# Performance work log

Hardware: AMD Instinct MI355X
Metric: run time of the kernel (lower is better)

The kernel has to match this reference:

```python
import jax, jax.numpy as jnp
import numpy as np

IN_F, OUT_F = 1024, 1024
NUM, K = 5, 3            # pykan defaults: num grid intervals, spline degree
X_RANGE = 1.0
LN_EPS = 1e-5
BATCH = 4096


def _make_grid():
    # pykan: linspace over [-R, R] with num+1 points, extended by k points of
    # uniform spacing h on each side -> (in_dim, num + 2k + 1)
    g = np.linspace(-X_RANGE, X_RANGE, NUM + 1)
    h = (g[-1] - g[0]) / NUM
    ext = np.concatenate([g[0] - h * np.arange(K, 0, -1), g, g[-1] + h * np.arange(1, K + 1)])
    grid = np.broadcast_to(ext, (IN_F, NUM + 2 * K + 1)).copy()
    return jnp.asarray(grid, dtype=jnp.float32)


def setup_inputs() -> dict:
    key = jax.random.key(0)
    ks = jax.random.split(key, 4)
    x = jax.random.uniform(ks[0], (BATCH, IN_F), jnp.float32, -1.0, 1.0)
    coef = jax.random.normal(ks[1], (IN_F, OUT_F, NUM + K), jnp.float32) * 0.1
    scale_base = jax.random.normal(ks[2], (IN_F, OUT_F), jnp.float32) / jnp.sqrt(jnp.float32(IN_F))
    scale_sp = jnp.ones((IN_F, OUT_F), jnp.float32)
    gamma = jnp.ones((OUT_F,), jnp.float32)   # LayerNorm weight
    beta = jnp.zeros((OUT_F,), jnp.float32)   # LayerNorm bias
    return {"x": x, "coef": coef, "scale_base": scale_base, "scale_sp": scale_sp,
            "gamma": gamma, "beta": beta, "grid": _make_grid()}


def _b_splines(x, grid, k):
    # Cox-de Boor recursion, exactly as pykan B_batch (uniform grid -> no NaNs).
    # x: (B, in), grid: (in, G) -> basis (B, in, NUM + k)
    xe = x[:, :, None]
    g = grid[None, :, :]
    B = ((xe >= g[:, :, :-1]) & (xe < g[:, :, 1:])).astype(x.dtype)
    for p in range(1, k + 1):
        B = ((xe - g[:, :, :-(p + 1)]) / (g[:, :, p:-1] - g[:, :, :-(p + 1)]) * B[:, :, :-1]
             + (g[:, :, p + 1:] - xe) / (g[:, :, p + 1:] - g[:, :, 1:-p]) * B[:, :, 1:])
    return B


def reference(x, coef, scale_base, scale_sp, gamma, beta, grid):
    basis = _b_splines(x, grid, K)                        # (B, in, NUM+K)
    spline = jnp.einsum('bik,iok->bio', basis, coef)      # (B, in, out)
    base = jax.nn.silu(x)                                 # (B, in)  pykan base_fun
    y = scale_base[None, :, :] * base[:, :, None] + scale_sp[None, :, :] * spline
    y = jnp.sum(y, axis=1)                                # (B, out)
    # LayerNorm(out_features)
    mu = jnp.mean(y, axis=-1, keepdims=True)
    var = jnp.var(y, axis=-1, keepdims=True)
    return (y - mu) * jax.lax.rsqrt(var + LN_EPS) * gamma + beta
```

## Files before the change

kernel.cpp:

```cpp
#include <hip/hip_runtime.h>

#define IN_F   1024
#define OUT_F  1024
#define BATCHN 4096
#define KDIM   9216

using i32x4 = __attribute__((ext_vector_type(4))) int;

__device__ __forceinline__ unsigned short f2bf(float f) {
  union { float f; unsigned int u; } v; v.f = f;
  unsigned int u = v.u;
  unsigned int r = (u + 0x7FFFu + ((u >> 16) & 1u)) >> 16;
  return (unsigned short)r;
}

__device__ __forceinline__ float bf2f(unsigned short h) {
  union { unsigned int u; float f; } v; v.u = ((unsigned int)h) << 16;
  return v.f;
}

#define ASCALE 172.0f

__device__ __forceinline__ unsigned char qa(float v) {
  return (unsigned char)(char)__float2int_rn(v * ASCALE);
}

__device__ __forceinline__ void async_load16(const void* g, void* l) {
  __builtin_amdgcn_global_load_lds(
      (__attribute__((address_space(1))) void*)(g),
      (__attribute__((address_space(3))) void*)(l),
      16, 0, 0);
}

__global__ __launch_bounds__(256) void kan_prep(const float* __restrict__ x,
                                                const float* __restrict__ grid,
                                                const float* __restrict__ sb,
                                                const float* __restrict__ ssp,
                                                const float* __restrict__ coef,
                                                unsigned char* __restrict__ A,
                                                unsigned int* __restrict__ sraw) {
  int bid = blockIdx.x;
  int tid = threadIdx.x;
  if (bid < 4096) {
    int idx4 = bid * 256 + tid;
    int b  = idx4 >> 8;
    int i0 = (idx4 & 255) * 4;
    const float4 xv4 = *(const float4*)(x + (size_t)b * IN_F + i0);
    const float4* gp = (const float4*)grid;
    float4 g0 = gp[0], g1 = gp[1], g2 = gp[2];
    float t[12] = {g0.x, g0.y, g0.z, g0.w, g1.x, g1.y, g1.z, g1.w,
                   g2.x, g2.y, g2.z, g2.w};
    float inv_h = 1.0f / (t[4] - t[3]);
    const float invp[3] = {inv_h, inv_h * 0.5f, inv_h * (1.0f / 3.0f)};
    float xs[4] = {xv4.x, xv4.y, xv4.z, xv4.w};
    unsigned char o9[9][4];
#pragma unroll
    for (int e = 0; e < 4; ++e) {
      float xv = xs[e];
      float sil = xv / (1.0f + __expf(-xv));
      float B[11];
#pragma unroll
      for (int j = 0; j < 11; ++j) B[j] = (xv >= t[j] && xv < t[j + 1]) ? 1.0f : 0.0f;
#pragma unroll
      for (int p = 1; p <= 3; ++p) {
        float ip = invp[p - 1];
#pragma unroll
        for (int j = 0; j + p < 11; ++j)
          B[j] = (xv - t[j]) * ip * B[j] + (t[j + p + 1] - xv) * ip * B[j + 1];
      }
      o9[0][e] = qa(sil);
#pragma unroll
      for (int k = 0; k < 8; ++k) o9[k + 1][e] = qa(B[k]);
    }
    size_t base = (size_t)b * KDIM + i0;
#pragma unroll
    for (int tp = 0; tp < 9; ++tp)
      *(unsigned int*)(A + base + (size_t)tp * 1024) = *(const unsigned int*)&o9[tp][0];
  } else {
    int b2 = bid - 4096;
    int o  = (b2 & 3) * 256 + tid;
    int ib = (b2 >> 2) * 32;
    float m = 0.f;
    for (int ii = 0; ii < 32; ++ii) {
      int io = (ib + ii) * 1024 + o;
      float s = ssp[io];
      float mm = fabsf(sb[io]);
      const float4* cp = (const float4*)(coef + (size_t)io * 8);
      float4 c0 = cp[0], c1 = cp[1];
      mm = fmaxf(mm, fmaxf(fmaxf(fabsf(s * c0.x), fabsf(s * c0.y)),
                           fmaxf(fabsf(s * c0.z), fabsf(s * c0.w))));
      mm = fmaxf(mm, fmaxf(fmaxf(fabsf(s * c1.x), fabsf(s * c1.y)),
                           fmaxf(fabsf(s * c1.z), fabsf(s * c1.w))));
      m = fmaxf(m, mm);
    }
    atomicMax(sraw + o, __float_as_uint(m));
  }
}

__global__ __launch_bounds__(256) void kan_prep_w(const float* __restrict__ sb,
                                                  const float* __restrict__ ssp,
                                                  const float* __restrict__ coef,
                                                  const unsigned int* __restrict__ sraw,
                                                  unsigned char* __restrict__ WT) {
  __shared__ unsigned char lds[9][128][33];
  int i0 = (blockIdx.x >> 5) * 128, o0 = (blockIdx.x & 31) * 32;
  int tid = threadIdx.x;
  int oo = tid & 31;
  float qs = 127.f / __uint_as_float(sraw[o0 + oo]);
#pragma unroll
  for (int r = 0; r < 16; ++r) {
    int idx = r * 256 + tid;
    int ii = idx >> 5;
    int io = (i0 + ii) * 1024 + (o0 + oo);
    float b = sb[io], s = ssp[io];
    const float4* cp = (const float4*)(coef + (size_t)io * 8);
    float4 c0 = cp[0], c1 = cp[1];
    lds[0][ii][oo] = (unsigned char)(char)__float2int_rn(b * qs);
    lds[1][ii][oo] = (unsigned char)(char)__float2int_rn(s * c0.x * qs);
    lds[2][ii][oo] = (unsigned char)(char)__float2int_rn(s * c0.y * qs);
    lds[3][ii][oo] = (unsigned char)(char)__float2int_rn(s * c0.z * qs);
    lds[4][ii][oo] = (unsigned char)(char)__float2int_rn(s * c0.w * qs);
    lds[5][ii][oo] = (unsigned char)(char)__float2int_rn(s * c1.x * qs);
    lds[6][ii][oo] = (unsigned char)(char)__float2int_rn(s * c1.y * qs);
    lds[7][ii][oo] = (unsigned char)(char)__float2int_rn(s * c1.z * qs);
    lds[8][ii][oo] = (unsigned char)(char)__float2int_rn(s * c1.w * qs);
  }
  __syncthreads();
  int woo = tid >> 3, ig = tid & 7;
  size_t rowbase = (size_t)(o0 + woo) * KDIM + i0 + ig * 16;
#pragma unroll
  for (int tp = 0; tp < 9; ++tp) {
    unsigned char tmp[16];
#pragma unroll
    for (int q = 0; q < 16; ++q) tmp[q] = lds[tp][ig * 16 + q][woo];
    *(uint4*)(WT + rowbase + (size_t)tp * 1024) = *(const uint4*)tmp;
  }
}

#define BM 256
#define BN 256
#define BKB 128
#define NSP 4
#define KQ   (KDIM / NSP)
#define NSLI (KQ / BKB)
#define SLOT 32768

__global__ __launch_bounds__(512, 2) void kan_gemm(const unsigned char* __restrict__ A,
                                                   const unsigned char* __restrict__ BT,
                                                   const unsigned int* __restrict__ sraw,
                                                   unsigned short* __restrict__ P) {
  extern __shared__ unsigned char lds[];
  unsigned char* As = lds;
  unsigned char* Bs = lds + 3 * SLOT;
  const int tid = threadIdx.x;
  const int wid = tid >> 6, lane = tid & 63;
  const int wr = wid >> 2, wc = wid & 3;
  const int row16 = lane & 15, kgrp = lane >> 4;
  const int rswB = (row16 & 7) << 4;

  int wg = ((blockIdx.x & 7) << 5) | (blockIdx.x >> 3);
  const int s = wg >> 6;
  const int m0 = ((wg >> 2) & 15) * BM, n0 = (wg & 3) * BN;
  const size_t kbase = (size_t)s * KQ;
  const unsigned char* Ab = A;
  const unsigned char* Bb = BT;

  i32x4 acc[8][4] = {};

  auto stage = [&](const unsigned char* Gb, int grow0, unsigned char* slotp, int sl) {
    size_t kbyte = kbase + (size_t)sl * BKB;
#pragma unroll
    for (int q = 0; q < 4; ++q) {
      int d = q * 8192 + tid * 16;
      int row = d >> 7;
      int csw = (d & 127) ^ ((row & 7) << 4);
      async_load16(Gb + (size_t)(grow0 + row) * KDIM + kbyte + csw,
                   slotp + (q * 8192 + wid * 1024));
    }
  };

  stage(Ab, m0, As, 0);
  stage(Bb, n0, Bs, 0);
  stage(Ab, m0, As + SLOT, 1);

  int consA = 0;
  for (int sl = 0; sl < NSLI; ++sl) {
    if (sl < NSLI - 1) asm volatile("s_waitcnt vmcnt(4)" ::: "memory");
    else               asm volatile("s_waitcnt vmcnt(0)" ::: "memory");
    __builtin_amdgcn_s_barrier();
    __builtin_amdgcn_sched_barrier(0);
    const unsigned char* as = As + consA * SLOT;
    const unsigned char* bs = Bs + (sl & 1) * SLOT;
    const int cb0 = (kgrp << 4) ^ rswB;
    const int cb1 = (64 | (kgrp << 4)) ^ rswB;

    i32x4 b0[4], a0[4];
#pragma unroll
    for (int n = 0; n < 4; ++n)
      b0[n] = *(const i32x4*)(bs + (wc * 64 + n * 16 + row16) * 128 + cb0);
#pragma unroll
    for (int m = 0; m < 4; ++m)
      a0[m] = *(const i32x4*)(as + (wr * 128 + m * 16 + row16) * 128 + cb0);
    if (sl + 1 < NSLI) stage(Bb, n0, Bs + ((sl + 1) & 1) * SLOT, sl + 1);
    __builtin_amdgcn_sched_barrier(0);
    __builtin_amdgcn_s_barrier();
    __builtin_amdgcn_s_setprio(1);
#pragma unroll
    for (int m = 0; m < 4; ++m)
#pragma unroll
      for (int n = 0; n < 4; ++n)
        acc[m][n] = __builtin_amdgcn_mfma_i32_16x16x64_i8(a0[m], b0[n], acc[m][n], 0, 0, 0);
    __builtin_amdgcn_s_setprio(0);

    i32x4 a1[4];
#pragma unroll
    for (int m = 0; m < 4; ++m)
      a1[m] = *(const i32x4*)(as + (wr * 128 + (m + 4) * 16 + row16) * 128 + cb0);
    {
      int stgA = consA - 1; if (stgA < 0) stgA += 3;
      if (sl + 2 < NSLI) stage(Ab, m0, As + stgA * SLOT, sl + 2);
    }
    __builtin_amdgcn_sched_barrier(0);
    __builtin_amdgcn_s_barrier();
    __builtin_amdgcn_s_setprio(1);
#pragma unroll
    for (int m = 0; m < 4; ++m)
#pragma unroll
      for (int n = 0; n < 4; ++n)
        acc[m + 4][n] = __builtin_amdgcn_mfma_i32_16x16x64_i8(a1[m], b0[n], acc[m + 4][n], 0, 0, 0);
    __builtin_amdgcn_s_setprio(0);

    i32x4 b1[4], a2[4];
#pragma unroll
    for (int n = 0; n < 4; ++n)
      b1[n] = *(const i32x4*)(bs + (wc * 64 + n * 16 + row16) * 128 + cb1);
#pragma unroll
    for (int m = 0; m < 4; ++m)
      a2[m] = *(const i32x4*)(as + (wr * 128 + m * 16 + row16) * 128 + cb1);
    __builtin_amdgcn_sched_barrier(0);
    __builtin_amdgcn_s_barrier();
    __builtin_amdgcn_s_setprio(1);
#pragma unroll
    for (int m = 0; m < 4; ++m)
#pragma unroll
      for (int n = 0; n < 4; ++n)
        acc[m][n] = __builtin_amdgcn_mfma_i32_16x16x64_i8(a2[m], b1[n], acc[m][n], 0, 0, 0);
    __builtin_amdgcn_s_setprio(0);

    i32x4 a3[4];
#pragma unroll
    for (int m = 0; m < 4; ++m)
      a3[m] = *(const i32x4*)(as + (wr * 128 + (m + 4) * 16 + row16) * 128 + cb1);
    __builtin_amdgcn_sched_barrier(0);
    __builtin_amdgcn_s_barrier();
    __builtin_amdgcn_s_setprio(1);
#pragma unroll
    for (int m = 0; m < 4; ++m)
#pragma unroll
      for (int n = 0; n < 4; ++n)
        acc[m + 4][n] = __builtin_amdgcn_mfma_i32_16x16x64_i8(a3[m], b1[n], acc[m + 4][n], 0, 0, 0);
    __builtin_amdgcn_s_setprio(0);

    consA = (consA == 2) ? 0 : consA + 1;
  }

  float dq[4];
#pragma unroll
  for (int n = 0; n < 4; ++n)
    dq[n] = __uint_as_float(sraw[n0 + wc * 64 + n * 16 + row16]) * (1.f / (ASCALE * 127.f));

  unsigned short* Pb = P + (size_t)s * BATCHN * OUT_F
                     + (size_t)(m0 + wr * 128) * OUT_F + n0 + wc * 64;
#pragma unroll
  for (int m = 0; m < 8; ++m)
#pragma unroll
    for (int n = 0; n < 4; ++n)
#pragma unroll
      for (int r = 0; r < 4; ++r)
        Pb[(size_t)(m * 16 + kgrp * 4 + r) * OUT_F + n * 16 + row16] =
            f2bf((float)acc[m][n][r] * dq[n]);
}

__global__ __launch_bounds__(256) void kan_ln(float* __restrict__ y,
                                              const unsigned short* __restrict__ P,
                                              const float* __restrict__ gamma,
                                              const float* __restrict__ beta) {
  __shared__ float ss[4], ssq[4];
  int tid = threadIdx.x;
  float4 v = {0.f, 0.f, 0.f, 0.f};
#pragma unroll
  for (int pp = 0; pp < NSP; ++pp) {
    const ushort4 pv = ((const ushort4*)(P + (size_t)pp * BATCHN * OUT_F
                                           + (size_t)blockIdx.x * OUT_F))[tid];
    v.x += bf2f(pv.x);
    v.y += bf2f(pv.y);
    v.z += bf2f(pv.z);
    v.w += bf2f(pv.w);
  }
  float s = v.x + v.y + v.z + v.w;
  float q = v.x * v.x + v.y * v.y + v.z * v.z + v.w * v.w;
#pragma unroll
  for (int off = 1; off < 64; off <<= 1) {
    s += __shfl_xor(s, off);
    q += __shfl_xor(q, off);
  }
  if ((tid & 63) == 0) { ss[tid >> 6] = s; ssq[tid >> 6] = q; }
  __syncthreads();
  float S = ss[0] + ss[1] + ss[2] + ss[3];
  float Q = ssq[0] + ssq[1] + ssq[2] + ssq[3];
  float mu  = S * (1.0f / OUT_F);
  float var = Q * (1.0f / OUT_F) - mu * mu;
  float inv = rsqrtf(var + 1e-5f);
  const float4 g  = ((const float4*)gamma)[tid];
  const float4 bt = ((const float4*)beta)[tid];
  float4 o;
  o.x = (v.x - mu) * inv * g.x + bt.x;
  o.y = (v.y - mu) * inv * g.y + bt.y;
  o.z = (v.z - mu) * inv * g.z + bt.z;
  o.w = (v.w - mu) * inv * g.w + bt.w;
  ((float4*)(y + (size_t)blockIdx.x * OUT_F))[tid] = o;
}

extern "C" void kernel_launch(void* const* d_in, const int* in_sizes, int n_in,
                              void* d_out, int out_size, void* d_ws, size_t ws_size,
                              hipStream_t stream) {
  const float* x     = (const float*)d_in[0];
  const float* coef  = (const float*)d_in[1];
  const float* sb    = (const float*)d_in[2];
  const float* ssp   = (const float*)d_in[3];
  const float* gamma = (const float*)d_in[4];
  const float* beta  = (const float*)d_in[5];
  const float* grid  = (const float*)d_in[6];

  const size_t a_bytes  = (size_t)BATCHN * KDIM;
  const size_t wt_bytes = (size_t)OUT_F * KDIM;
  const size_t sr_bytes = 4096;
  const size_t p_bytes  = (size_t)NSP * BATCHN * OUT_F * 2;
  if (ws_size < a_bytes + wt_bytes + sr_bytes + p_bytes) return;

  unsigned char* A    = (unsigned char*)d_ws;
  unsigned char* WT   = A + a_bytes;
  unsigned int*  sraw = (unsigned int*)(WT + wt_bytes);
  unsigned short* P   = (unsigned short*)((unsigned char*)sraw + sr_bytes);
  float* y = (float*)d_out;

  const size_t lds_bytes = 5 * (size_t)SLOT;
  static bool attr_set = false;
  if (!attr_set) {
    hipFuncSetAttribute((const void*)kan_gemm,
                        hipFuncAttributeMaxDynamicSharedMemorySize, (int)lds_bytes);
    attr_set = true;
  }

  hipMemsetAsync(sraw, 0, sr_bytes, stream);
  kan_prep<<<dim3(4096 + 128), dim3(256), 0, stream>>>(x, grid, sb, ssp, coef, A, sraw);
  kan_prep_w<<<dim3((IN_F / 128) * (OUT_F / 32)), dim3(256), 0, stream>>>(sb, ssp, coef, sraw, WT);
  kan_gemm<<<dim3(NSP * (BATCHN / BM) * (OUT_F / BN)), dim3(512), lds_bytes, stream>>>(A, WT, sraw, P);
  kan_ln<<<dim3(BATCHN), dim3(256), 0, stream>>>(y, P, gamma, beta);
}
```

Measured before the change: 93.50 us.

## Fuse per-column weight max reduction into weight quantization kernel, drop atomics

The column-wise max used for int8 weight scaling moves out of the combined prep kernel and into the weight-quantization kernel. Each 512-thread block now owns 8 output columns, reduces their max over all inputs through shared memory, then quantizes and writes the transposed rows directly without an LDS transpose. This removes the memset, the global atomicMax and the cross-kernel dependency on sraw, and splits activation prep into its own kernel. The cost is that the weight kernel now runs only 128 blocks, which may underuse the GPU's bandwidth. Each block also reads its weight slice twice, relying on cache reuse for the second pass.

```diff
diff --git a/kernel.cpp b/kernel.cpp
--- a/kernel.cpp
+++ b/kernel.cpp
@@ -32,109 +32,103 @@
       16, 0, 0);
 }
 
-__global__ __launch_bounds__(256) void kan_prep(const float* __restrict__ x,
-                                                const float* __restrict__ grid,
-                                                const float* __restrict__ sb,
-                                                const float* __restrict__ ssp,
-                                                const float* __restrict__ coef,
-                                                unsigned char* __restrict__ A,
-                                                unsigned int* __restrict__ sraw) {
-  int bid = blockIdx.x;
-  int tid = threadIdx.x;
-  if (bid < 4096) {
-    int idx4 = bid * 256 + tid;
-    int b  = idx4 >> 8;
-    int i0 = (idx4 & 255) * 4;
-    const float4 xv4 = *(const float4*)(x + (size_t)b * IN_F + i0);
-    const float4* gp = (const float4*)grid;
-    float4 g0 = gp[0], g1 = gp[1], g2 = gp[2];
-    float t[12] = {g0.x, g0.y, g0.z, g0.w, g1.x, g1.y, g1.z, g1.w,
-                   g2.x, g2.y, g2.z, g2.w};
-    float inv_h = 1.0f / (t[4] - t[3]);
-    const float invp[3] = {inv_h, inv_h * 0.5f, inv_h * (1.0f / 3.0f)};
-    float xs[4] = {xv4.x, xv4.y, xv4.z, xv4.w};
-    unsigned char o9[9][4];
-#pragma unroll
-    for (int e = 0; e < 4; ++e) {
-      float xv = xs[e];
-      float sil = xv / (1.0f + __expf(-xv));
-      float B[11];
-#pragma unroll
-      for (int j = 0; j < 11; ++j) B[j] = (xv >= t[j] && xv < t[j + 1]) ? 1.0f : 0.0f;
-#pragma unroll
-      for (int p = 1; p <= 3; ++p) {
-        float ip = invp[p - 1];
-#pragma unroll
-        for (int j = 0; j + p < 11; ++j)
-          B[j] = (xv - t[j]) * ip * B[j] + (t[j + p + 1] - xv) * ip * B[j + 1];
-      }
-      o9[0][e] = qa(sil);
-#pragma unroll
-      for (int k = 0; k < 8; ++k) o9[k + 1][e] = qa(B[k]);
+__global__ __launch_bounds__(256) void kan_prep_a(const float* __restrict__ x,
+                                                  const float* __restrict__ grid,
+                                                  unsigned char* __restrict__ A) {
+  int idx4 = blockIdx.x * 256 + threadIdx.x;
+  int b  = idx4 >> 8;
+  int i0 = (idx4 & 255) * 4;
+  const float4 xv4 = *(const float4*)(x + (size_t)b * IN_F + i0);
+  const float4* gp = (const float4*)grid;
+  float4 g0 = gp[0], g1 = gp[1], g2 = gp[2];
+  float t[12] = {g0.x, g0.y, g0.z, g0.w, g1.x, g1.y, g1.z, g1.w,
+                 g2.x, g2.y, g2.z, g2.w};
+  float inv_h = 1.0f / (t[4] - t[3]);
+  const float invp[3] = {inv_h, inv_h * 0.5f, inv_h * (1.0f / 3.0f)};
+  float xs[4] = {xv4.x, xv4.y, xv4.z, xv4.w};
+  unsigned char o9[9][4];
+#pragma unroll
+  for (int e = 0; e < 4; ++e) {
+    float xv = xs[e];
+    float sil = xv / (1.0f + __expf(-xv));
+    float B[11];
+#pragma unroll
+    for (int j = 0; j < 11; ++j) B[j] = (xv >= t[j] && xv < t[j + 1]) ? 1.0f : 0.0f;
+#pragma unroll
+    for (int p = 1; p <= 3; ++p) {
+      float ip = invp[p - 1];
+#pragma unroll
+      for (int j = 0; j + p < 11; ++j)
+        B[j] = (xv - t[j]) * ip * B[j] + (t[j + p + 1] - xv) * ip * B[j + 1];
     }
-    size_t base = (size_t)b * KDIM + i0;
-#pragma unroll
-    for (int tp = 0; tp < 9; ++tp)
-      *(unsigned int*)(A + base + (size_t)tp * 1024) = *(const unsigned int*)&o9[tp][0];
-  } else {
-    int b2 = bid - 4096;
-    int o  = (b2 & 3) * 256 + tid;
-    int ib = (b2 >> 2) * 32;
-    float m = 0.f;
-    for (int ii = 0; ii < 32; ++ii) {
-      int io = (ib + ii) * 1024 + o;
-      float s = ssp[io];
-      float mm = fabsf(sb[io]);
-      const float4* cp = (const float4*)(coef + (size_t)io * 8);
-      float4 c0 = cp[0], c1 = cp[1];
-      mm = fmaxf(mm, fmaxf(fmaxf(fabsf(s * c0.x), fabsf(s * c0.y)),
-                           fmaxf(fabsf(s * c0.z), fabsf(s * c0.w))));
-      mm = fmaxf(mm, fmaxf(fmaxf(fabsf(s * c1.x), fabsf(s * c1.y)),
-                           fmaxf(fabsf(s * c1.z), fabsf(s * c1.w))));
-      m = fmaxf(m, mm);
-    }
-    atomicMax(sraw + o, __float_as_uint(m));
-  }
-}
-
-__global__ __launch_bounds__(256) void kan_prep_w(const float* __restrict__ sb,
+    o9[0][e] = qa(sil);
+#pragma unroll
+    for (int k = 0; k < 8; ++k) o9[k + 1][e] = qa(B[k]);
+  }
+  size_t base = (size_t)b * KDIM + i0;
+#pragma unroll
+  for (int tp = 0; tp < 9; ++tp)
+    *(unsigned int*)(A + base + (size_t)tp * 1024) = *(const unsigned int*)&o9[tp][0];
+}
+
+__global__ __launch_bounds__(512) void kan_prep_w(const float* __restrict__ sb,
                                                   const float* __restrict__ ssp,
                                                   const float* __restrict__ coef,
-                                                  const unsigned int* __restrict__ sraw,
+                                                  unsigned int* __restrict__ sraw,
                                                   unsigned char* __restrict__ WT) {
-  __shared__ unsigned char lds[9][128][33];
-  int i0 = (blockIdx.x >> 5) * 128, o0 = (blockIdx.x & 31) * 32;
-  int tid = threadIdx.x;
-  int oo = tid & 31;
-  float qs = 127.f / __uint_as_float(sraw[o0 + oo]);
-#pragma unroll
-  for (int r = 0; r < 16; ++r) {
-    int idx = r * 256 + tid;
-    int ii = idx >> 5;
-    int io = (i0 + ii) * 1024 + (o0 + oo);
+  __shared__ float lmax[64][8];
+  __shared__ float qs8[8];
+  const int tid = threadIdx.x;
+  const int oo = tid & 7, ig = tid >> 3;
+  const int o = blockIdx.x * 8 + oo;
+  const int ibase = ig * 16;
+
+  float m = 0.f;
+#pragma unroll 4
+  for (int ii = 0; ii < 16; ++ii) {
+    int io = (ibase + ii) * 1024 + o;
+    float s = ssp[io];
+    float mm = fabsf(sb[io]);
+    const float4* cp = (const float4*)(coef + (size_t)io * 8);
+    float4 c0 = cp[0], c1 = cp[1];
+    mm = fmaxf(mm, fmaxf(fmaxf(fabsf(s * c0.x), fabsf(s * c0.y)),
+                         fmaxf(fabsf(s * c0.z), fabsf(s * c0.w))));
+    mm = fmaxf(mm, fmaxf(fmaxf(fabsf(s * c1.x), fabsf(s * c1.y)),
+                         fmaxf(fabsf(s * c1.z), fabsf(s * c1.w))));
+    m = fmaxf(m, mm);
+  }
+  lmax[ig][oo] = m;
+  __syncthreads();
+  if (tid < 8) {
+    float mo = 0.f;
+    for (int r = 0; r < 64; ++r) mo = fmaxf(mo, lmax[r][tid]);
+    sraw[blockIdx.x * 8 + tid] = __float_as_uint(mo);
+    qs8[tid] = 127.f / mo;
+  }
+  __syncthreads();
+  const float qs = qs8[oo];
+
+  unsigned char tmp[9][16];
+#pragma unroll
+  for (int ii = 0; ii < 16; ++ii) {
+    int io = (ibase + ii) * 1024 + o;
     float b = sb[io], s = ssp[io];
     const float4* cp = (const float4*)(coef + (size_t)io * 8);
     float4 c0 = cp[0], c1 = cp[1];
-    lds[0][ii][oo] = (unsigned char)(char)__float2int_rn(b * qs);
-    lds[1][ii][oo] = (unsigned char)(char)__float2int_rn(s * c0.x * qs);
-    lds[2][ii][oo] = (unsigned char)(char)__float2int_rn(s * c0.y * qs);
-    lds[3][ii][oo] = (unsigned char)(char)__float2int_rn(s * c0.z * qs);
-    lds[4][ii][oo] = (unsigned char)(char)__float2int_rn(s * c0.w * qs);
-    lds[5][ii][oo] = (unsigned char)(char)__float2int_rn(s * c1.x * qs);
-    lds[6][ii][oo] = (unsigned char)(char)__float2int_rn(s * c1.y * qs);
-    lds[7][ii][oo] = (unsigned char)(char)__float2int_rn(s * c1.z * qs);
-    lds[8][ii][oo] = (unsigned char)(char)__float2int_rn(s * c1.w * qs);
-  }
-  __syncthreads();
-  int woo = tid >> 3, ig = tid & 7;
-  size_t rowbase = (size_t)(o0 + woo) * KDIM + i0 + ig * 16;
-#pragma unroll
-  for (int tp = 0; tp < 9; ++tp) {
-    unsigned char tmp[16];
-#pragma unroll
-    for (int q = 0; q < 16; ++q) tmp[q] = lds[tp][ig * 16 + q][woo];
-    *(uint4*)(WT + rowbase + (size_t)tp * 1024) = *(const uint4*)tmp;
-  }
+    tmp[0][ii] = (unsigned char)(char)__float2int_rn(b * qs);
+    tmp[1][ii] = (unsigned char)(char)__float2int_rn(s * c0.x * qs);
+    tmp[2][ii] = (unsigned char)(char)__float2int_rn(s * c0.y * qs);
+    tmp[3][ii] = (unsigned char)(char)__float2int_rn(s * c0.z * qs);
+    tmp[4][ii] = (unsigned char)(char)__float2int_rn(s * c0.w * qs);
+    tmp[5][ii] = (unsigned char)(char)__float2int_rn(s * c1.x * qs);
+    tmp[6][ii] = (unsigned char)(char)__float2int_rn(s * c1.y * qs);
+    tmp[7][ii] = (unsigned char)(char)__float2int_rn(s * c1.z * qs);
+    tmp[8][ii] = (unsigned char)(char)__float2int_rn(s * c1.w * qs);
+  }
+  size_t rowbase = (size_t)o * KDIM + ibase;
+#pragma unroll
+  for (int tp = 0; tp < 9; ++tp)
+    *(uint4*)(WT + rowbase + (size_t)tp * 1024) = *(const uint4*)&tmp[tp][0];
 }
 
 #define BM 256
@@ -352,9 +346,8 @@
     attr_set = true;
   }
 
-  hipMemsetAsync(sraw, 0, sr_bytes, stream);
-  kan_prep<<<dim3(4096 + 128), dim3(256), 0, stream>>>(x, grid, sb, ssp, coef, A, sraw);
-  kan_prep_w<<<dim3((IN_F / 128) * (OUT_F / 32)), dim3(256), 0, stream>>>(sb, ssp, coef, sraw, WT);
+  kan_prep_a<<<dim3((BATCHN * IN_F) / 1024), dim3(256), 0, stream>>>(x, grid, A);
+  kan_prep_w<<<dim3(OUT_F / 8), dim3(512), 0, stream>>>(sb, ssp, coef, sraw, WT);
   kan_gemm<<<dim3(NSP * (BATCHN / BM) * (OUT_F / BN)), dim3(512), lds_bytes, stream>>>(A, WT, sraw, P);
   kan_ln<<<dim3(BATCHN), dim3(256), 0, stream>>>(y, P, gamma, beta);
 }
```

Measured after the change: 96.66 us. 3.4% more time.
